# Kernel optimization log

Measured on AMD Instinct MI355X. Metric: run time of the kernel, lower is better.

The kernel has to match this reference:

```python
import jax, jax.numpy as jnp
import numpy as np

N = 50000      # nodes
E = 800000     # edges
DN = 128       # input node feature dim
D = 64         # dim_embed
H = 2          # attention heads (layer 0)
NEG_SLOPE = 0.2
LN_EPS = 1e-5


def setup_inputs() -> dict:
    key = jax.random.key(0)
    ks = jax.random.split(key, 10)
    s = 0.1  # weight scale
    return {
        "h":  jax.random.normal(ks[0], (N, DN), jnp.float32),
        "W0": jax.random.normal(ks[1], (DN, H * D), jnp.float32) * s,
        "al0": jax.random.normal(ks[2], (H, D), jnp.float32) * s,
        "ar0": jax.random.normal(ks[3], (H, D), jnp.float32) * s,
        "b0": jnp.zeros((H * D,), jnp.float32),
        "W1": jax.random.normal(ks[4], (H * D, D), jnp.float32) * s,
        "al1": jax.random.normal(ks[5], (1, D), jnp.float32) * s,
        "ar1": jax.random.normal(ks[6], (1, D), jnp.float32) * s,
        "b1": jnp.zeros((D,), jnp.float32),
        "g0": jnp.ones((H * D,), jnp.float32),
        "be0": jnp.zeros((H * D,), jnp.float32),
        "g1": jnp.ones((D,), jnp.float32),
        "be1": jnp.zeros((D,), jnp.float32),
        "src": jax.random.randint(ks[7], (E,), 0, N, jnp.int32),
        "dst": jax.random.randint(ks[8], (E,), 0, N, jnp.int32),
    }


def layer_norm(x, g, b):
    mu = jnp.mean(x, axis=-1, keepdims=True)
    var = jnp.mean(jnp.square(x - mu), axis=-1, keepdims=True)
    return (x - mu) * jax.lax.rsqrt(var + LN_EPS) * g + b


def gat_conv(h, W, attn_l, attn_r, bias, src, dst, heads, dim):
    # DGL GATConv (feat_drop=attn_drop=0, allow_zero_in_degree=True, bias=True)
    feat = (h @ W).reshape(-1, heads, dim)            # [N, H, D]
    el = jnp.einsum("nhd,hd->nh", feat, attn_l)       # [N, H]
    er = jnp.einsum("nhd,hd->nh", feat, attn_r)       # [N, H]
    e = jax.nn.leaky_relu(el[src] + er[dst], NEG_SLOPE)  # [E, H]
    # segment softmax over incoming edges of each dst node
    m = jax.ops.segment_max(e, dst, num_segments=N)      # [N, H]
    p = jnp.exp(e - m[dst])                              # [E, H]
    denom = jax.ops.segment_sum(p, dst, num_segments=N)  # [N, H]
    alpha = p / denom[dst]                               # [E, H]
    msg = feat[src] * alpha[:, :, None]                  # [E, H, D]
    rst = jax.ops.segment_sum(msg, dst, num_segments=N)  # [N, H, D]
    return rst + bias.reshape(1, heads, dim)


def reference(h, W0, al0, ar0, b0, W1, al1, ar1, b1, g0, be0, g1, be1, src, dst):
    # layer 0: H heads, relu(flatten), layer norm
    x = gat_conv(h, W0, al0, ar0, b0, src, dst, H, D)     # [N, H, D]
    x = jax.nn.relu(x.reshape(N, H * D))
    x = layer_norm(x, g0, be0)
    # layer 1: 1 head, mean over heads (== squeeze), layer norm
    y = gat_conv(x, W1, al1, ar1, b1, src, dst, 1, D)     # [N, 1, D]
    y = jnp.mean(y, axis=1)                               # [N, D]
    return layer_norm(y, g1, be1)
```

## Files before the change

### kernel.cpp

```cpp
#include <hip/hip_runtime.h>
#include <hip/hip_bf16.h>


#define NN 50000
#define EE 800000
#define NBUCK 196
#define CHUNK 4096
#define CAP 8192
#define NBBIN 196
#define ELS_CAP 1024

typedef _Float16 h2 __attribute__((ext_vector_type(2)));
typedef _Float16 h4 __attribute__((ext_vector_type(4)));
typedef _Float16 h8 __attribute__((ext_vector_type(8)));
typedef float f32x4 __attribute__((ext_vector_type(4)));

__device__ __forceinline__ h2 i2h(int v) { union { int i; h2 h; } u; u.i = v; return u.h; }
__device__ __forceinline__ int h2i(h2 v) { union { h2 h; int i; } u; u.h = v; return u.i; }

#define SEL_LO 0x01000504u
#define SEL_HI 0x03020706u

__global__ __launch_bounds__(1024) void k_init(
    const float* __restrict__ W0, const float* __restrict__ W1,
    h8* __restrict__ Wp0, h8* __restrict__ Wp1, int* __restrict__ bcntp)
{
    int tid = threadIdx.x;
    int b = blockIdx.x;
    if (b < 2) {
        int idx = b * 1024 + tid;
        int lane = idx & 63, kk = (idx >> 6) & 3, tt = idx >> 8;
        int q = lane >> 4, c = lane & 15;
        h8 v;
#pragma unroll
        for (int j = 0; j < 8; ++j)
            v[j] = (_Float16)W0[(kk * 32 + q * 8 + j) * 128 + tt * 16 + c];
        Wp0[idx] = v;
    } else if (b == 2) {
        int idx = tid;
        int lane = idx & 63, kk = (idx >> 6) & 3, tt = idx >> 8;
        int q = lane >> 4, c = lane & 15;
        h8 v;
#pragma unroll
        for (int j = 0; j < 8; ++j)
            v[j] = (_Float16)W1[(kk * 32 + q * 8 + j) * 64 + tt * 16 + c];
        Wp1[idx] = v;
    } else {
        for (int i = tid; i < NBUCK * 16; i += 1024) bcntp[i] = 0;
    }
}

#define HS_STRIDE 136
#define D0_STRIDE 132
__global__ __launch_bounds__(1024) void k_work(
    const int* __restrict__ src, const int* __restrict__ dst,
    int* __restrict__ bcntp, unsigned int* __restrict__ staging,
    const float* __restrict__ h, const h8* __restrict__ Wp0,
    const float* __restrict__ al0, const float* __restrict__ ar0,
    _Float16* __restrict__ feat0, float* __restrict__ el0, float* __restrict__ er0)
{
    int tid = threadIdx.x;
    __shared__ char smem[64 * D0_STRIDE * 4];
    __shared__ int hist[NBUCK];
    __shared__ int rnk[NBUCK];
    __shared__ int gbase[NBUCK];
    if (blockIdx.x < NBBIN) {
        int base = blockIdx.x * CHUNK;
        int m = EE - base; if (m > CHUNK) m = CHUNK;
        if (tid < NBUCK) { hist[tid] = 0; rnk[tid] = 0; }
        __syncthreads();
        int e0 = tid * 4;
        bool act = e0 < m;
        int4 d4 = {0, 0, 0, 0}, s4 = {0, 0, 0, 0};
        if (act) {
            d4 = ((const int4*)(dst + base))[tid];
            s4 = ((const int4*)(src + base))[tid];
            atomicAdd(&hist[d4.x >> 8], 1);
            atomicAdd(&hist[d4.y >> 8], 1);
            atomicAdd(&hist[d4.z >> 8], 1);
            atomicAdd(&hist[d4.w >> 8], 1);
        }
        __syncthreads();
        if (tid < NBUCK && hist[tid])
            gbase[tid] = atomicAdd(&bcntp[tid * 16], hist[tid]);
        __syncthreads();
        if (act) {
            int d[4] = {d4.x, d4.y, d4.z, d4.w};
            int s[4] = {s4.x, s4.y, s4.z, s4.w};
#pragma unroll
            for (int k = 0; k < 4; ++k) {
                int b = d[k] >> 8;
                int r = atomicAdd(&rnk[b], 1);
                int slot = gbase[b] + r;
                if (slot < CAP)
                    staging[(size_t)b * CAP + slot] =
                        ((unsigned)(d[k] & 255) << 16) | (unsigned)s[k];
            }
        }
        return;
    }
    _Float16* hs = (_Float16*)smem;
    float* ds2 = (float*)smem;
    int n0 = (blockIdx.x - NBBIN) * 64;
#pragma unroll
    for (int r = 0; r < 2; ++r) {
        int f = tid + 1024 * r;
        int node = f >> 5, kc = f & 31;
        int n = n0 + node;
        float4 v = {0.f, 0.f, 0.f, 0.f};
        if (n < NN) v = ((const float4*)h)[(size_t)n * 32 + kc];
        h4 hv; hv[0] = (_Float16)v.x; hv[1] = (_Float16)v.y;
        hv[2] = (_Float16)v.z; hv[3] = (_Float16)v.w;
        *(h4*)&hs[node * HS_STRIDE + kc * 4] = hv;
    }
    __syncthreads();
    int w16 = tid >> 6, lane = tid & 63;
    int rg = w16 & 3, tt = w16 >> 2;
    int m = lane & 15, q = lane >> 4;
    h8 aF[4];
#pragma unroll
    for (int kk = 0; kk < 4; ++kk)
        aF[kk] = *(const h8*)&hs[(rg * 16 + m) * HS_STRIDE + kk * 32 + q * 8];
    __syncthreads();
#pragma unroll
    for (int t2 = 0; t2 < 2; ++t2) {
        int t = tt * 2 + t2;
        f32x4 acc = {0.f, 0.f, 0.f, 0.f};
#pragma unroll
        for (int kk = 0; kk < 4; ++kk) {
            h8 bF = Wp0[(t * 4 + kk) * 64 + lane];
            acc = __builtin_amdgcn_mfma_f32_16x16x32_f16(aF[kk], bF, acc, 0, 0, 0);
        }
#pragma unroll
        for (int r = 0; r < 4; ++r)
            ds2[(rg * 16 + q * 4 + r) * D0_STRIDE + t * 16 + m] = acc[r];
    }
    __syncthreads();
    {
        int node = tid >> 4, c8 = tid & 15;
        int n = n0 + node;
        if (n < NN) {
            float4 a = *(const float4*)&ds2[node * D0_STRIDE + c8 * 8];
            float4 b = *(const float4*)&ds2[node * D0_STRIDE + c8 * 8 + 4];
            h8 v;
            v[0] = (_Float16)a.x; v[1] = (_Float16)a.y; v[2] = (_Float16)a.z; v[3] = (_Float16)a.w;
            v[4] = (_Float16)b.x; v[5] = (_Float16)b.y; v[6] = (_Float16)b.z; v[7] = (_Float16)b.w;
            ((h8*)feat0)[(size_t)n * 16 + c8] = v;
        }
    }
    if (tid < 256) {
        int node = tid >> 2, qq = tid & 3;
        int n = n0 + node;
        float pl = 0.f, pr = 0.f;
#pragma unroll
        for (int i = 0; i < 8; ++i) {
            float4 v = *(const float4*)&ds2[node * D0_STRIDE + qq * 32 + i * 4];
            float4 a = ((const float4*)al0)[qq * 8 + i];
            float4 r = ((const float4*)ar0)[qq * 8 + i];
            pl += v.x * a.x + v.y * a.y + v.z * a.z + v.w * a.w;
            pr += v.x * r.x + v.y * r.y + v.z * r.z + v.w * r.w;
        }
        pl += __shfl_xor(pl, 1, 4); pr += __shfl_xor(pr, 1, 4);
        if (n < NN) {
            if (qq == 0) { el0[n * 2] = pl;     er0[n * 2] = pr; }
            if (qq == 2) { el0[n * 2 + 1] = pl; er0[n * 2 + 1] = pr; }
        }
    }
}

__global__ __launch_bounds__(256) void k_final(
    const unsigned int* __restrict__ staging, const int* __restrict__ bcntp,
    int* __restrict__ off, unsigned short* __restrict__ ssort)
{
    int b = blockIdx.x;
    int tid = threadIdx.x;
    int cnt = bcntp[b * 16]; if (cnt > CAP) cnt = CAP;
    size_t base = (size_t)b * CAP;
    __shared__ unsigned short buf[CAP];
    __shared__ int hist[256];
    __shared__ int sc[256];
    int bv = (tid < NBUCK) ? bcntp[tid * 16] : 0;
    sc[tid] = bv;
    __syncthreads();
    for (int o = 1; o < 256; o <<= 1) {
        int u = (tid >= o) ? sc[tid - o] : 0;
        __syncthreads();
        sc[tid] += u;
        __syncthreads();
    }
    int lo = (b > 0) ? sc[b - 1] : 0;
    if (b == 0 && tid == 0) off[0] = 0;
    __syncthreads();
    hist[tid] = 0;
    __syncthreads();
    for (int i = tid; i < cnt; i += 256)
        atomicAdd(&hist[staging[base + i] >> 16], 1);
    __syncthreads();
    int hv = hist[tid];
    sc[tid] = hv;
    __syncthreads();
    for (int o = 1; o < 256; o <<= 1) {
        int u = (tid >= o) ? sc[tid - o] : 0;
        __syncthreads();
        sc[tid] += u;
        __syncthreads();
    }
    int nlo = b << 8;
    int nrem = NN - nlo; if (nrem > 256) nrem = 256;
    if (tid < nrem) off[nlo + tid + 1] = lo + sc[tid];
    hist[tid] = sc[tid] - hv;
    __syncthreads();
    for (int i = tid; i < cnt; i += 256) {
        unsigned rec = staging[base + i];
        int r = atomicAdd(&hist[rec >> 16], 1);
        buf[r] = (unsigned short)(rec & 0xFFFFu);
    }
    __syncthreads();
    for (int i = tid; i < cnt; i += 256)
        ssort[lo + i] = buf[i];
}

#define D1_STRIDE 68
__global__ __launch_bounds__(512) void k_aggemm(
    const int* __restrict__ off, const unsigned short* __restrict__ ssort,
    const float* __restrict__ el0, const float* __restrict__ er0,
    const _Float16* __restrict__ feat0, const float* __restrict__ b0,
    const float* __restrict__ g0, const float* __restrict__ be0,
    const h8* __restrict__ Wp1, const float* __restrict__ al1,
    const float* __restrict__ ar1,
    _Float16* __restrict__ feat1, float* __restrict__ el1, float* __restrict__ er1)
{
    int tid = threadIdx.x;
    int w8 = tid >> 6, lane = tid & 63;
    int g = lane >> 4, c = lane & 15;
    int n0 = blockIdx.x * 32;
    __shared__ char smem[32 * HS_STRIDE * 2 > 32 * D1_STRIDE * 4
                         ? 32 * HS_STRIDE * 2 : 32 * D1_STRIDE * 4];
    __shared__ int2 esc[8][4][18];
    __shared__ uint2 els[ELS_CAP];
    _Float16* xs = (_Float16*)smem;
    float* ds2 = (float*)smem;
    const int4* fb = (const int4*)feat0;
    const float2* el0f2 = (const float2*)el0;
    unsigned qsel = (c < 8) ? SEL_LO : SEL_HI;
    int blo = off[n0];
    int nhi = n0 + 32; if (nhi > NN) nhi = NN;
    int bhi = off[nhi];
    int bcnt = bhi - blo; if (bcnt > ELS_CAP) bcnt = ELS_CAP;
    for (int e = tid; e < bcnt; e += 512) {
        int s = ssort[blo + e];
        float2 el = el0f2[s];
        h2 ep; ep[0] = (_Float16)el.x; ep[1] = (_Float16)el.y;
        els[e] = make_uint2((unsigned)s, (unsigned)h2i(ep));
    }
    __syncthreads();
    {
        int nl = w8 * 4 + g;
        int n = n0 + nl;
        if (n < NN) {
            int beg = off[n], end = off[n + 1];
            float2 ern2 = ((const float2*)er0)[n];
            float acc[8] = {};
            float den0 = 0.f, den1 = 0.f;
            for (int cb = beg; cb < end; cb += 16) {
                int m = end - cb; if (m > 16) m = 16;
                int s_reg = 0; float p0 = 0.f, p1 = 0.f;
                if (c < m) {
                    int idx = cb + c - blo;
                    uint2 rec;
                    if (idx < ELS_CAP) rec = els[idx];
                    else {
                        int s = ssort[cb + c];
                        float2 el = el0f2[s];
                        h2 ep; ep[0] = (_Float16)el.x; ep[1] = (_Float16)el.y;
                        rec = make_uint2((unsigned)s, (unsigned)h2i(ep));
                    }
                    s_reg = (int)rec.x;
                    h2 ep = i2h((int)rec.y);
                    float v0 = (float)ep[0] + ern2.x; v0 = v0 > 0.f ? v0 : 0.2f * v0;
                    float v1 = (float)ep[1] + ern2.y; v1 = v1 > 0.f ? v1 : 0.2f * v1;
                    p0 = __expf(v0); p1 = __expf(v1);
                }
                den0 += p0; den1 += p1;
                h2 pp; pp[0] = (_Float16)p0; pp[1] = (_Float16)p1;
                esc[w8][g][c] = make_int2(s_reg, h2i(pp));
                for (int ii = 0; ii < m; ii += 2) {
                    int4 rr = *(const int4*)&esc[w8][g][ii];
                    int qp = __builtin_amdgcn_perm(rr.y, rr.w, qsel);
                    int4 iA = fb[(size_t)rr.x * 16 + c];
                    int4 iB = fb[(size_t)rr.z * 16 + c];
                    h2 q2 = i2h(qp);
                    int pe, po;
                    pe = __builtin_amdgcn_perm(iA.x, iB.x, SEL_LO);
                    po = __builtin_amdgcn_perm(iA.x, iB.x, SEL_HI);
                    acc[0] = __builtin_amdgcn_fdot2(i2h(pe), q2, acc[0], false);
                    acc[1] = __builtin_amdgcn_fdot2(i2h(po), q2, acc[1], false);
                    pe = __builtin_amdgcn_perm(iA.y, iB.y, SEL_LO);
                    po = __builtin_amdgcn_perm(iA.y, iB.y, SEL_HI);
                    acc[2] = __builtin_amdgcn_fdot2(i2h(pe), q2, acc[2], false);
                    acc[3] = __builtin_amdgcn_fdot2(i2h(po), q2, acc[3], false);
                    pe = __builtin_amdgcn_perm(iA.z, iB.z, SEL_LO);
                    po = __builtin_amdgcn_perm(iA.z, iB.z, SEL_HI);
                    acc[4] = __builtin_amdgcn_fdot2(i2h(pe), q2, acc[4], false);
                    acc[5] = __builtin_amdgcn_fdot2(i2h(po), q2, acc[5], false);
                    pe = __builtin_amdgcn_perm(iA.w, iB.w, SEL_LO);
                    po = __builtin_amdgcn_perm(iA.w, iB.w, SEL_HI);
                    acc[6] = __builtin_amdgcn_fdot2(i2h(pe), q2, acc[6], false);
                    acc[7] = __builtin_amdgcn_fdot2(i2h(po), q2, acc[7], false);
                }
            }
#pragma unroll
            for (int o = 1; o < 16; o <<= 1) {
                den0 += __shfl_xor(den0, o, 16);
                den1 += __shfl_xor(den1, o, 16);
            }
            float den = (c < 8) ? den0 : den1;
            float inv = (end > beg) ? 1.f / den : 0.f;
            float4 ba = ((const float4*)b0)[c * 2];
            float4 bb = ((const float4*)b0)[c * 2 + 1];
            float val[8];
            val[0] = fmaxf(acc[0] * inv + ba.x, 0.f);
            val[1] = fmaxf(acc[1] * inv + ba.y, 0.f);
            val[2] = fmaxf(acc[2] * inv + ba.z, 0.f);
            val[3] = fmaxf(acc[3] * inv + ba.w, 0.f);
            val[4] = fmaxf(acc[4] * inv + bb.x, 0.f);
            val[5] = fmaxf(acc[5] * inv + bb.y, 0.f);
            val[6] = fmaxf(acc[6] * inv + bb.z, 0.f);
            val[7] = fmaxf(acc[7] * inv + bb.w, 0.f);
            float s1 = 0.f, s2 = 0.f;
#pragma unroll
            for (int k = 0; k < 8; ++k) { s1 += val[k]; s2 += val[k] * val[k]; }
#pragma unroll
            for (int o = 1; o < 16; o <<= 1) { s1 += __shfl_xor(s1, o, 16); s2 += __shfl_xor(s2, o, 16); }
            float mu = s1 * (1.f / 128.f);
            float var = s2 * (1.f / 128.f) - mu * mu;
            float rs = rsqrtf(var + 1e-5f);
            float4 ga = ((const float4*)g0)[c * 2];
            float4 gb = ((const float4*)g0)[c * 2 + 1];
            float4 ea = ((const float4*)be0)[c * 2];
            float4 eb = ((const float4*)be0)[c * 2 + 1];
            h8 xv;
            xv[0] = (_Float16)((val[0] - mu) * rs * ga.x + ea.x);
            xv[1] = (_Float16)((val[1] - mu) * rs * ga.y + ea.y);
            xv[2] = (_Float16)((val[2] - mu) * rs * ga.z + ea.z);
            xv[3] = (_Float16)((val[3] - mu) * rs * ga.w + ea.w);
            xv[4] = (_Float16)((val[4] - mu) * rs * gb.x + eb.x);
            xv[5] = (_Float16)((val[5] - mu) * rs * gb.y + eb.y);
            xv[6] = (_Float16)((val[6] - mu) * rs * gb.z + eb.z);
            xv[7] = (_Float16)((val[7] - mu) * rs * gb.w + eb.w);
            *(h8*)&xs[nl * HS_STRIDE + c * 8] = xv;
        } else {
            h8 z = {};
            *(h8*)&xs[nl * HS_STRIDE + c * 8] = z;
        }
    }
    __syncthreads();
    int rg = w8 & 1, t = w8 >> 1;
    int m = lane & 15, q = lane >> 4;
    h8 aF[4];
#pragma unroll
    for (int kk = 0; kk < 4; ++kk)
        aF[kk] = *(const h8*)&xs[(rg * 16 + m) * HS_STRIDE + kk * 32 + q * 8];
    __syncthreads();
    f32x4 acc1 = {0.f, 0.f, 0.f, 0.f};
#pragma unroll
    for (int kk = 0; kk < 4; ++kk) {
        h8 bF = Wp1[(t * 4 + kk) * 64 + lane];
        acc1 = __builtin_amdgcn_mfma_f32_16x16x32_f16(aF[kk], bF, acc1, 0, 0, 0);
    }
#pragma unroll
    for (int r = 0; r < 4; ++r)
        ds2[(rg * 16 + q * 4 + r) * D1_STRIDE + t * 16 + m] = acc1[r];
    __syncthreads();
    if (tid < 256) {
        int node = tid >> 3, c8 = tid & 7;
        int n = n0 + node;
        if (n < NN) {
            float4 a = *(const float4*)&ds2[node * D1_STRIDE + c8 * 8];
            float4 b = *(const float4*)&ds2[node * D1_STRIDE + c8 * 8 + 4];
            h8 v;
            v[0] = (_Float16)a.x; v[1] = (_Float16)a.y; v[2] = (_Float16)a.z; v[3] = (_Float16)a.w;
            v[4] = (_Float16)b.x; v[5] = (_Float16)b.y; v[6] = (_Float16)b.z; v[7] = (_Float16)b.w;
            ((h8*)feat1)[(size_t)n * 8 + c8] = v;
        }
    } else if (tid < 384) {
        int t2 = tid - 256;
        int node = t2 >> 2, qq = t2 & 3;
        int n = n0 + node;
        float pl = 0.f, pr = 0.f;
#pragma unroll
        for (int i = 0; i < 4; ++i) {
            float4 v = *(const float4*)&ds2[node * D1_STRIDE + qq * 16 + i * 4];
            float4 a = ((const float4*)al1)[qq * 4 + i];
            float4 r = ((const float4*)ar1)[qq * 4 + i];
            pl += v.x * a.x + v.y * a.y + v.z * a.z + v.w * a.w;
            pr += v.x * r.x + v.y * r.y + v.z * r.z + v.w * r.w;
        }
        pl += __shfl_xor(pl, 1, 4); pr += __shfl_xor(pr, 1, 4);
        pl += __shfl_xor(pl, 2, 4); pr += __shfl_xor(pr, 2, 4);
        if (qq == 0 && n < NN) { el1[n] = pl; er1[n] = pr; }
    }
}

__global__ __launch_bounds__(256) void k_agg1(
    const int* __restrict__ off, const unsigned short* __restrict__ ssort,
    const float* __restrict__ el1, const float* __restrict__ er1,
    const _Float16* __restrict__ feat1, const float* __restrict__ b1,
    const float* __restrict__ g1, const float* __restrict__ be1,
    float* __restrict__ out)
{
    int tid = threadIdx.x;
    int w = tid >> 6, lane = tid & 63;
    int g = lane >> 3, c = lane & 7;
    int n0 = blockIdx.x * 32;
    int n = n0 + w * 8 + g;
    __shared__ int2 esc[4][8][10];
    __shared__ uint2 els[ELS_CAP];
    const int4* fb = (const int4*)feat1;
    int blo = off[n0];
    int nhi = n0 + 32; if (nhi > NN) nhi = NN;
    int bhi = off[nhi];
    int bcnt = bhi - blo; if (bcnt > ELS_CAP) bcnt = ELS_CAP;
    for (int e = tid; e < bcnt; e += 256) {
        int s = ssort[blo + e];
        els[e] = make_uint2((unsigned)s, (unsigned)__float_as_int(el1[s]));
    }
    __syncthreads();
    if (n >= NN) return;
    int beg = off[n], end = off[n + 1];
    float ern = er1[n];
    float acc[8] = {};
    float den = 0.f;
    for (int cb = beg; cb < end; cb += 8) {
        int m = end - cb; if (m > 8) m = 8;
        int s_reg = 0; float p_reg = 0.f;
        if (c < m) {
            int idx = cb + c - blo;
            uint2 rec;
            if (idx < ELS_CAP) rec = els[idx];
            else {
                int s = ssort[cb + c];
                rec = make_uint2((unsigned)s, (unsigned)__float_as_int(el1[s]));
            }
            s_reg = (int)rec.x;
            float v = __int_as_float((int)rec.y) + ern;
            v = v > 0.f ? v : 0.2f * v;
            p_reg = __expf(v);
        }
        den += p_reg;
        h2 pp; pp[0] = (_Float16)p_reg; pp[1] = (_Float16)0.f;
        esc[w][g][c] = make_int2(s_reg, h2i(pp));
        for (int ii = 0; ii < m; ii += 2) {
            int4 rr = *(const int4*)&esc[w][g][ii];
            int qp = __builtin_amdgcn_perm(rr.y, rr.w, SEL_LO);
            int4 iA = fb[(size_t)rr.x * 8 + c];
            int4 iB = fb[(size_t)rr.z * 8 + c];
            h2 q2 = i2h(qp);
            int pe, po;
            pe = __builtin_amdgcn_perm(iA.x, iB.x, SEL_LO);
            po = __builtin_amdgcn_perm(iA.x, iB.x, SEL_HI);
            acc[0] = __builtin_amdgcn_fdot2(i2h(pe), q2, acc[0], false);
            acc[1] = __builtin_amdgcn_fdot2(i2h(po), q2, acc[1], false);
            pe = __builtin_amdgcn_perm(iA.y, iB.y, SEL_LO);
            po = __builtin_amdgcn_perm(iA.y, iB.y, SEL_HI);
            acc[2] = __builtin_amdgcn_fdot2(i2h(pe), q2, acc[2], false);
            acc[3] = __builtin_amdgcn_fdot2(i2h(po), q2, acc[3], false);
            pe = __builtin_amdgcn_perm(iA.z, iB.z, SEL_LO);
            po = __builtin_amdgcn_perm(iA.z, iB.z, SEL_HI);
            acc[4] = __builtin_amdgcn_fdot2(i2h(pe), q2, acc[4], false);
            acc[5] = __builtin_amdgcn_fdot2(i2h(po), q2, acc[5], false);
            pe = __builtin_amdgcn_perm(iA.w, iB.w, SEL_LO);
            po = __builtin_amdgcn_perm(iA.w, iB.w, SEL_HI);
            acc[6] = __builtin_amdgcn_fdot2(i2h(pe), q2, acc[6], false);
            acc[7] = __builtin_amdgcn_fdot2(i2h(po), q2, acc[7], false);
        }
    }
#pragma unroll
    for (int o = 1; o < 8; o <<= 1) den += __shfl_xor(den, o, 8);
    float inv = (end > beg) ? 1.f / den : 0.f;
    float4 ba = ((const float4*)b1)[c * 2];
    float4 bb = ((const float4*)b1)[c * 2 + 1];
    float val[8];
    val[0] = acc[0] * inv + ba.x; val[1] = acc[1] * inv + ba.y;
    val[2] = acc[2] * inv + ba.z; val[3] = acc[3] * inv + ba.w;
    val[4] = acc[4] * inv + bb.x; val[5] = acc[5] * inv + bb.y;
    val[6] = acc[6] * inv + bb.z; val[7] = acc[7] * inv + bb.w;
    float s1 = 0.f, s2 = 0.f;
#pragma unroll
    for (int k = 0; k < 8; ++k) { s1 += val[k]; s2 += val[k] * val[k]; }
#pragma unroll
    for (int o = 1; o < 8; o <<= 1) { s1 += __shfl_xor(s1, o, 8); s2 += __shfl_xor(s2, o, 8); }
    float mu = s1 * (1.f / 64.f);
    float var = s2 * (1.f / 64.f) - mu * mu;
    float rs = rsqrtf(var + 1e-5f);
    float4 ga = ((const float4*)g1)[c * 2];
    float4 gb = ((const float4*)g1)[c * 2 + 1];
    float4 ea = ((const float4*)be1)[c * 2];
    float4 eb = ((const float4*)be1)[c * 2 + 1];
    float4 oa, ob;
    oa.x = (val[0] - mu) * rs * ga.x + ea.x;
    oa.y = (val[1] - mu) * rs * ga.y + ea.y;
    oa.z = (val[2] - mu) * rs * ga.z + ea.z;
    oa.w = (val[3] - mu) * rs * ga.w + ea.w;
    ob.x = (val[4] - mu) * rs * gb.x + eb.x;
    ob.y = (val[5] - mu) * rs * gb.y + eb.y;
    ob.z = (val[6] - mu) * rs * gb.z + eb.z;
    ob.w = (val[7] - mu) * rs * gb.w + eb.w;
    float4* orow = (float4*)(out + (size_t)n * 64);
    orow[c * 2] = oa;
    orow[c * 2 + 1] = ob;
}

extern "C" void kernel_launch(void* const* d_in, const int* in_sizes, int n_in,
                              void* d_out, int out_size, void* d_ws, size_t ws_size,
                              hipStream_t stream)
{
    const float* h   = (const float*)d_in[0];
    const float* W0  = (const float*)d_in[1];
    const float* al0 = (const float*)d_in[2];
    const float* ar0 = (const float*)d_in[3];
    const float* b0  = (const float*)d_in[4];
    const float* W1  = (const float*)d_in[5];
    const float* al1 = (const float*)d_in[6];
    const float* ar1 = (const float*)d_in[7];
    const float* b1  = (const float*)d_in[8];
    const float* g0  = (const float*)d_in[9];
    const float* be0 = (const float*)d_in[10];
    const float* g1  = (const float*)d_in[11];
    const float* be1 = (const float*)d_in[12];
    const int*   src = (const int*)d_in[13];
    const int*   dst = (const int*)d_in[14];
    float* out = (float*)d_out;

    char* p = (char*)d_ws;
    auto alloc = [&](size_t bytes) -> char* {
        char* r = p;
        p += (bytes + 255) & ~(size_t)255;
        return r;
    };
    _Float16* feat0 = (_Float16*)alloc((size_t)NN * 128 * sizeof(_Float16));
    float* el0   = (float*)alloc((size_t)NN * 2 * sizeof(float));
    float* er0   = (float*)alloc((size_t)NN * 2 * sizeof(float));
    _Float16* feat1 = (_Float16*)alloc((size_t)NN * 64 * sizeof(_Float16));
    float* el1   = (float*)alloc((size_t)NN * sizeof(float));
    float* er1   = (float*)alloc((size_t)NN * sizeof(float));
    int*   bcntp = (int*)alloc((size_t)NBUCK * 16 * sizeof(int));
    int*   off   = (int*)alloc((size_t)(NN + 1) * sizeof(int));
    unsigned int*   staging = (unsigned int*)alloc((size_t)NBUCK * CAP * sizeof(unsigned int));
    unsigned short* ssort   = (unsigned short*)alloc((size_t)EE * sizeof(unsigned short));
    h8*    Wp0   = (h8*)alloc(2048 * sizeof(h8));
    h8*    Wp1   = (h8*)alloc(1024 * sizeof(h8));

    const int GB0 = (NN + 63) / 64;
    k_init<<<4, 1024, 0, stream>>>(W0, W1, Wp0, Wp1, bcntp);
    k_work<<<NBBIN + GB0, 1024, 0, stream>>>(src, dst, bcntp, staging,
                                             h, Wp0, al0, ar0, feat0, el0, er0);
    k_final<<<NBUCK, 256, 0, stream>>>(staging, bcntp, off, ssort);
    k_aggemm<<<(NN + 31) / 32, 512, 0, stream>>>(off, ssort, el0, er0, feat0,
                                                 b0, g0, be0, Wp1, al1, ar1,
                                                 feat1, el1, er1);
    k_agg1<<<(NN + 31) / 32, 256, 0, stream>>>(off, ssort, el1, er1, feat1,
                                               b1, g1, be1, out);
}
```

Before: 183.0 us.

## Regroup launches: fuse weight packing into binning, merge bucket sort with GEMM

Restructures the pre-aggregation kernels. A memset zeroes the bucket counters. Weight packing moves into the edge-binning kernel as extra blocks. The per-bucket counting sort, widened to 1024 threads, runs as extra blocks inside the layer-0 GEMM kernel instead of as its own launch. This removes one kernel launch and lets the sort overlap the dense GEMM blocks, but the binning now sits alone in its own kernel and the sort uses 1024-thread blocks where most threads sit idle during the scans.

New measurement: 177.4 us. 3.1% less time.

```diff
diff --git a/kernel.cpp b/kernel.cpp
--- a/kernel.cpp
+++ b/kernel.cpp
@@ -21,87 +21,136 @@
 #define SEL_LO 0x01000504u
 #define SEL_HI 0x03020706u
 
-__global__ __launch_bounds__(1024) void k_init(
+__global__ __launch_bounds__(1024) void k_bin(
+    const int* __restrict__ src, const int* __restrict__ dst,
+    int* __restrict__ bcntp, unsigned int* __restrict__ staging,
     const float* __restrict__ W0, const float* __restrict__ W1,
-    h8* __restrict__ Wp0, h8* __restrict__ Wp1, int* __restrict__ bcntp)
+    h8* __restrict__ Wp0, h8* __restrict__ Wp1)
 {
     int tid = threadIdx.x;
-    int b = blockIdx.x;
-    if (b < 2) {
-        int idx = b * 1024 + tid;
-        int lane = idx & 63, kk = (idx >> 6) & 3, tt = idx >> 8;
-        int q = lane >> 4, c = lane & 15;
-        h8 v;
-#pragma unroll
-        for (int j = 0; j < 8; ++j)
-            v[j] = (_Float16)W0[(kk * 32 + q * 8 + j) * 128 + tt * 16 + c];
-        Wp0[idx] = v;
-    } else if (b == 2) {
-        int idx = tid;
-        int lane = idx & 63, kk = (idx >> 6) & 3, tt = idx >> 8;
-        int q = lane >> 4, c = lane & 15;
-        h8 v;
-#pragma unroll
-        for (int j = 0; j < 8; ++j)
-            v[j] = (_Float16)W1[(kk * 32 + q * 8 + j) * 64 + tt * 16 + c];
-        Wp1[idx] = v;
-    } else {
-        for (int i = tid; i < NBUCK * 16; i += 1024) bcntp[i] = 0;
+    if (blockIdx.x >= NBBIN) {
+        int wb = blockIdx.x - NBBIN;
+        if (wb < 2) {
+            int idx = wb * 1024 + tid;
+            int lane = idx & 63, kk = (idx >> 6) & 3, tt = idx >> 8;
+            int q = lane >> 4, c = lane & 15;
+            h8 v;
+#pragma unroll
+            for (int j = 0; j < 8; ++j)
+                v[j] = (_Float16)W0[(kk * 32 + q * 8 + j) * 128 + tt * 16 + c];
+            Wp0[idx] = v;
+        } else {
+            int idx = tid;
+            int lane = idx & 63, kk = (idx >> 6) & 3, tt = idx >> 8;
+            int q = lane >> 4, c = lane & 15;
+            h8 v;
+#pragma unroll
+            for (int j = 0; j < 8; ++j)
+                v[j] = (_Float16)W1[(kk * 32 + q * 8 + j) * 64 + tt * 16 + c];
+            Wp1[idx] = v;
+        }
+        return;
+    }
+    __shared__ int hist[NBUCK];
+    __shared__ int rnk[NBUCK];
+    __shared__ int gbase[NBUCK];
+    int base = blockIdx.x * CHUNK;
+    int m = EE - base; if (m > CHUNK) m = CHUNK;
+    if (tid < NBUCK) { hist[tid] = 0; rnk[tid] = 0; }
+    __syncthreads();
+    int e0 = tid * 4;
+    bool act = e0 < m;
+    int4 d4 = {0, 0, 0, 0}, s4 = {0, 0, 0, 0};
+    if (act) {
+        d4 = ((const int4*)(dst + base))[tid];
+        s4 = ((const int4*)(src + base))[tid];
+        atomicAdd(&hist[d4.x >> 8], 1);
+        atomicAdd(&hist[d4.y >> 8], 1);
+        atomicAdd(&hist[d4.z >> 8], 1);
+        atomicAdd(&hist[d4.w >> 8], 1);
+    }
+    __syncthreads();
+    if (tid < NBUCK && hist[tid])
+        gbase[tid] = atomicAdd(&bcntp[tid * 16], hist[tid]);
+    __syncthreads();
+    if (act) {
+        int d[4] = {d4.x, d4.y, d4.z, d4.w};
+        int s[4] = {s4.x, s4.y, s4.z, s4.w};
+#pragma unroll
+        for (int k = 0; k < 4; ++k) {
+            int b = d[k] >> 8;
+            int r = atomicAdd(&rnk[b], 1);
+            int slot = gbase[b] + r;
+            if (slot < CAP)
+                staging[(size_t)b * CAP + slot] =
+                    ((unsigned)(d[k] & 255) << 16) | (unsigned)s[k];
+        }
     }
 }
 
 #define HS_STRIDE 136
 #define D0_STRIDE 132
-__global__ __launch_bounds__(1024) void k_work(
-    const int* __restrict__ src, const int* __restrict__ dst,
-    int* __restrict__ bcntp, unsigned int* __restrict__ staging,
+__global__ __launch_bounds__(1024) void k_mid(
+    const unsigned int* __restrict__ staging, const int* __restrict__ bcntp,
+    int* __restrict__ off, unsigned short* __restrict__ ssort,
     const float* __restrict__ h, const h8* __restrict__ Wp0,
     const float* __restrict__ al0, const float* __restrict__ ar0,
     _Float16* __restrict__ feat0, float* __restrict__ el0, float* __restrict__ er0)
 {
     int tid = threadIdx.x;
     __shared__ char smem[64 * D0_STRIDE * 4];
-    __shared__ int hist[NBUCK];
-    __shared__ int rnk[NBUCK];
-    __shared__ int gbase[NBUCK];
-    if (blockIdx.x < NBBIN) {
-        int base = blockIdx.x * CHUNK;
-        int m = EE - base; if (m > CHUNK) m = CHUNK;
-        if (tid < NBUCK) { hist[tid] = 0; rnk[tid] = 0; }
-        __syncthreads();
-        int e0 = tid * 4;
-        bool act = e0 < m;
-        int4 d4 = {0, 0, 0, 0}, s4 = {0, 0, 0, 0};
-        if (act) {
-            d4 = ((const int4*)(dst + base))[tid];
-            s4 = ((const int4*)(src + base))[tid];
-            atomicAdd(&hist[d4.x >> 8], 1);
-            atomicAdd(&hist[d4.y >> 8], 1);
-            atomicAdd(&hist[d4.z >> 8], 1);
-            atomicAdd(&hist[d4.w >> 8], 1);
-        }
-        __syncthreads();
-        if (tid < NBUCK && hist[tid])
-            gbase[tid] = atomicAdd(&bcntp[tid * 16], hist[tid]);
-        __syncthreads();
-        if (act) {
-            int d[4] = {d4.x, d4.y, d4.z, d4.w};
-            int s[4] = {s4.x, s4.y, s4.z, s4.w};
-#pragma unroll
-            for (int k = 0; k < 4; ++k) {
-                int b = d[k] >> 8;
-                int r = atomicAdd(&rnk[b], 1);
-                int slot = gbase[b] + r;
-                if (slot < CAP)
-                    staging[(size_t)b * CAP + slot] =
-                        ((unsigned)(d[k] & 255) << 16) | (unsigned)s[k];
-            }
-        }
+    if (blockIdx.x < NBUCK) {
+        int b = blockIdx.x;
+        int cnt = bcntp[b * 16]; if (cnt > CAP) cnt = CAP;
+        size_t base = (size_t)b * CAP;
+        unsigned short* buf = (unsigned short*)smem;
+        __shared__ int hist[256];
+        __shared__ int sc[256];
+        if (tid < 256) sc[tid] = (tid < NBUCK) ? bcntp[tid * 16] : 0;
+        __syncthreads();
+        for (int o = 1; o < 256; o <<= 1) {
+            int u = 0;
+            if (tid < 256 && tid >= o) u = sc[tid - o];
+            __syncthreads();
+            if (tid < 256) sc[tid] += u;
+            __syncthreads();
+        }
+        int lo = (b > 0) ? sc[b - 1] : 0;
+        if (b == 0 && tid == 0) off[0] = 0;
+        __syncthreads();
+        if (tid < 256) hist[tid] = 0;
+        __syncthreads();
+        for (int i = tid; i < cnt; i += 1024)
+            atomicAdd(&hist[staging[base + i] >> 16], 1);
+        __syncthreads();
+        int hv = (tid < 256) ? hist[tid] : 0;
+        if (tid < 256) sc[tid] = hv;
+        __syncthreads();
+        for (int o = 1; o < 256; o <<= 1) {
+            int u = 0;
+            if (tid < 256 && tid >= o) u = sc[tid - o];
+            __syncthreads();
+            if (tid < 256) sc[tid] += u;
+            __syncthreads();
+        }
+        int nlo = b << 8;
+        int nrem = NN - nlo; if (nrem > 256) nrem = 256;
+        if (tid < nrem) off[nlo + tid + 1] = lo + sc[tid];
+        if (tid < 256) hist[tid] = sc[tid] - hv;
+        __syncthreads();
+        for (int i = tid; i < cnt; i += 1024) {
+            unsigned rec = staging[base + i];
+            int r = atomicAdd(&hist[rec >> 16], 1);
+            buf[r] = (unsigned short)(rec & 0xFFFFu);
+        }
+        __syncthreads();
+        for (int i = tid; i < cnt; i += 1024)
+            ssort[lo + i] = buf[i];
         return;
     }
     _Float16* hs = (_Float16*)smem;
     float* ds2 = (float*)smem;
-    int n0 = (blockIdx.x - NBBIN) * 64;
+    int n0 = (blockIdx.x - NBUCK) * 64;
 #pragma unroll
     for (int r = 0; r < 2; ++r) {
         int f = tid + 1024 * r;
@@ -166,58 +215,6 @@
             if (qq == 2) { el0[n * 2 + 1] = pl; er0[n * 2 + 1] = pr; }
         }
     }
-}
-
-__global__ __launch_bounds__(256) void k_final(
-    const unsigned int* __restrict__ staging, const int* __restrict__ bcntp,
-    int* __restrict__ off, unsigned short* __restrict__ ssort)
-{
-    int b = blockIdx.x;
-    int tid = threadIdx.x;
-    int cnt = bcntp[b * 16]; if (cnt > CAP) cnt = CAP;
-    size_t base = (size_t)b * CAP;
-    __shared__ unsigned short buf[CAP];
-    __shared__ int hist[256];
-    __shared__ int sc[256];
-    int bv = (tid < NBUCK) ? bcntp[tid * 16] : 0;
-    sc[tid] = bv;
-    __syncthreads();
-    for (int o = 1; o < 256; o <<= 1) {
-        int u = (tid >= o) ? sc[tid - o] : 0;
-        __syncthreads();
-        sc[tid] += u;
-        __syncthreads();
-    }
-    int lo = (b > 0) ? sc[b - 1] : 0;
-    if (b == 0 && tid == 0) off[0] = 0;
-    __syncthreads();
-    hist[tid] = 0;
-    __syncthreads();
-    for (int i = tid; i < cnt; i += 256)
-        atomicAdd(&hist[staging[base + i] >> 16], 1);
-    __syncthreads();
-    int hv = hist[tid];
-    sc[tid] = hv;
-    __syncthreads();
-    for (int o = 1; o < 256; o <<= 1) {
-        int u = (tid >= o) ? sc[tid - o] : 0;
-        __syncthreads();
-        sc[tid] += u;
-        __syncthreads();
-    }
-    int nlo = b << 8;
-    int nrem = NN - nlo; if (nrem > 256) nrem = 256;
-    if (tid < nrem) off[nlo + tid + 1] = lo + sc[tid];
-    hist[tid] = sc[tid] - hv;
-    __syncthreads();
-    for (int i = tid; i < cnt; i += 256) {
-        unsigned rec = staging[base + i];
-        int r = atomicAdd(&hist[rec >> 16], 1);
-        buf[r] = (unsigned short)(rec & 0xFFFFu);
-    }
-    __syncthreads();
-    for (int i = tid; i < cnt; i += 256)
-        ssort[lo + i] = buf[i];
 }
 
 #define D1_STRIDE 68
@@ -552,10 +549,10 @@
     h8*    Wp1   = (h8*)alloc(1024 * sizeof(h8));
 
     const int GB0 = (NN + 63) / 64;
-    k_init<<<4, 1024, 0, stream>>>(W0, W1, Wp0, Wp1, bcntp);
-    k_work<<<NBBIN + GB0, 1024, 0, stream>>>(src, dst, bcntp, staging,
-                                             h, Wp0, al0, ar0, feat0, el0, er0);
-    k_final<<<NBUCK, 256, 0, stream>>>(staging, bcntp, off, ssort);
+    hipMemsetAsync(bcntp, 0, (size_t)NBUCK * 16 * sizeof(int), stream);
+    k_bin<<<NBBIN + 3, 1024, 0, stream>>>(src, dst, bcntp, staging, W0, W1, Wp0, Wp1);
+    k_mid<<<NBUCK + GB0, 1024, 0, stream>>>(staging, bcntp, off, ssort,
+                                            h, Wp0, al0, ar0, feat0, el0, er0);
     k_aggemm<<<(NN + 31) / 32, 512, 0, stream>>>(off, ssort, el0, er0, feat0,
                                                  b0, g0, be0, Wp1, al1, ar1,
                                                  feat1, el1, er1);
```
